# Performance work log

Measured on AMD Instinct MI355X. Metric: run time of the kernel, lower is better.

## Reference

```python
import jax, jax.numpy as jnp
import numpy as np


def lut_quantize(v, lut):
    """Nearest-neighbor LUT quantization with straight-through estimator.
    lut is sorted ascending; uses searchsorted (no [N, L] blowup)."""
    L = lut.shape[0]
    idx = jnp.clip(jnp.searchsorted(lut, v), 1, L - 1)
    left = jnp.take(lut, idx - 1)
    right = jnp.take(lut, idx)
    q = jnp.where(v - left <= right - v, left, right)
    return v + jax.lax.stop_gradient(q - v)


def mem_conv(x, w, b, lut):
    # memConv2d: weights/bias snapped to LUT levels, then standard 3x3 SAME conv (NCHW/OIHW)
    wq = lut_quantize(w, lut)
    bq = lut_quantize(b, lut)
    y = jax.lax.conv_general_dilated(x, wq, window_strides=(1, 1),
                                     padding=((1, 1), (1, 1)),
                                     dimension_numbers=('NCHW', 'OIHW', 'NCHW'))
    return y + bq[None, :, None, None]


def mem_linear(x, w, b, lut):
    # memLinear: torch-style weight (out, in)
    return x @ lut_quantize(w, lut).T + lut_quantize(b, lut)


def mem_relu(x, lut):
    # memReLu: ReLU followed by LUT quantization of the activation
    return lut_quantize(jnp.maximum(x, 0.0), lut)


def max_pool_2x2(x):
    return jax.lax.reduce_window(x, -jnp.inf, jax.lax.max,
                                 (1, 1, 2, 2), (1, 1, 2, 2), 'VALID')


def _forward(x, lut, w1, b1, w2, b2, w3, b3, w4, b4, w5, b5, w6, b6,
             fw1, fb1, fw2, fb2, fw3, fb3):
    x = mem_relu(mem_conv(x, w1, b1, lut), lut)
    x = mem_relu(mem_conv(x, w2, b2, lut), lut)
    x = max_pool_2x2(x)                      # [B,32,16,16]
    x = mem_relu(mem_conv(x, w3, b3, lut), lut)
    x = mem_relu(mem_conv(x, w4, b4, lut), lut)
    x = max_pool_2x2(x)                      # [B,64,8,8]
    x = mem_relu(mem_conv(x, w5, b5, lut), lut)
    x = mem_relu(mem_conv(x, w6, b6, lut), lut)
    x = max_pool_2x2(x)                      # [B,128,4,4]
    x = x.reshape(-1, 128 * 4 * 4)
    x = mem_relu(mem_linear(x, fw1, fb1, lut), lut)
    x = mem_relu(mem_linear(x, fw2, fb2, lut), lut)
    x = mem_linear(x, fw3, fb3, lut)
    return jax.nn.softmax(x, axis=1)


def setup_inputs() -> dict:
    key = jax.random.key(0)
    ks = jax.random.split(key, 20)
    B = 512
    lut = jnp.linspace(-4.0, 4.0, 129).astype(jnp.float32)

    def conv_w(k, co, ci):
        scale = np.sqrt(2.0 / (ci * 9)).astype(np.float32)
        return jax.random.normal(k, (co, ci, 3, 3), jnp.float32) * scale

    def lin_w(k, co, ci):
        scale = np.sqrt(2.0 / ci).astype(np.float32)
        return jax.random.normal(k, (co, ci), jnp.float32) * scale

    return {
        'x': jax.random.normal(ks[0], (B, 3, 32, 32), jnp.float32),
        'lut': lut,
        'w1': conv_w(ks[1], 32, 3),   'b1': jnp.zeros((32,), jnp.float32),
        'w2': conv_w(ks[2], 32, 32),  'b2': jnp.zeros((32,), jnp.float32),
        'w3': conv_w(ks[3], 64, 32),  'b3': jnp.zeros((64,), jnp.float32),
        'w4': conv_w(ks[4], 64, 64),  'b4': jnp.zeros((64,), jnp.float32),
        'w5': conv_w(ks[5], 128, 64), 'b5': jnp.zeros((128,), jnp.float32),
        'w6': conv_w(ks[6], 128, 128),'b6': jnp.zeros((128,), jnp.float32),
        'fw1': lin_w(ks[7], 512, 2048), 'fb1': jnp.zeros((512,), jnp.float32),
        'fw2': lin_w(ks[8], 128, 512),  'fb2': jnp.zeros((128,), jnp.float32),
        'fw3': lin_w(ks[9], 10, 128),   'fb3': jnp.zeros((10,), jnp.float32),
    }


def reference(x, lut, w1, b1, w2, b2, w3, b3, w4, b4, w5, b5, w6, b6,
              fw1, fb1, fw2, fb2, fw3, fb3):
    return _forward(x, lut, w1, b1, w2, b2, w3, b3, w4, b4, w5, b5, w6, b6,
                    fw1, fb1, fw2, fb2, fw3, fb3)
```

## Files before the change

kernel.cpp:

```cpp
#include <hip/hip_runtime.h>
#include <cstddef>


#define B_SZ 512
typedef unsigned int u32;
typedef __attribute__((ext_vector_type(4))) int i32x4;

__device__ __forceinline__ float lutq(float v) {
    float k = ceilf(v * 16.0f - 0.5f);
    k = fminf(64.0f, fmaxf(-64.0f, k));
    return k * 0.0625f;
}
__device__ __forceinline__ int kq(float x) {
    float kf = ceilf(x * 16.0f - 0.5f);
    kf = fminf(64.0f, fmaxf(-64.0f, kf));
    return (int)kf;
}
__device__ __forceinline__ u32 bmax4u(u32 a, u32 b) {
    u32 r = 0;
    #pragma unroll
    for (int j = 0; j < 4; ++j) {
        u32 x = (a >> (8 * j)) & 255u, y = (b >> (8 * j)) & 255u;
        r |= (x > y ? x : y) << (8 * j);
    }
    return r;
}

__device__ __forceinline__ void prep_conv_frag(const float* __restrict__ w, char* __restrict__ q,
                                               int i, int CI) {
    int NSTEP = (9 * CI + 63) / 64;
    int e = i & 15, t = i >> 4;
    int ln = t & 63, t2 = t >> 6;
    int s = t2 % NSTEP, co_tile = t2 / NSTEP;
    int k = s * 64 + ((ln >> 4) << 4) + e;
    int tap = k / CI, ci = k % CI;
    int co = co_tile * 16 + (ln & 15);
    int val = 0;
    if (tap < 9) val = kq(w[(co * CI + ci) * 9 + tap]);
    q[i] = (char)val;
}
__device__ __forceinline__ void prep_fc_frag(const float* __restrict__ w, char* __restrict__ q,
                                             int i, int K) {
    int S = K >> 6;
    int e = i & 15, t = i >> 4;
    int ln = t & 63, t2 = t >> 6;
    int s = t2 % S, n_tile = t2 / S;
    int n = n_tile * 16 + (ln & 15);
    int k = s * 64 + ((ln >> 4) << 4) + e;
    q[i] = (char)kq(w[(size_t)n * K + k]);
}

__global__ __launch_bounds__(256) void prep_weights(
    const float* __restrict__ w2, const float* __restrict__ w3, const float* __restrict__ w4,
    const float* __restrict__ w5, const float* __restrict__ w6,
    const float* __restrict__ fw1, const float* __restrict__ fw2,
    char* q2, char* q3, char* q4, char* q5, char* q6, char* qf1, char* qf2)
{
    int i = blockIdx.x * 256 + threadIdx.x;
    if (i < 10240)                  { prep_conv_frag(w2, q2, i, 32);  }
    else if ((i -= 10240) < 20480)  { prep_conv_frag(w3, q3, i, 32);  }
    else if ((i -= 20480) < 36864)  { prep_conv_frag(w4, q4, i, 64);  }
    else if ((i -= 36864) < 73728)  { prep_conv_frag(w5, q5, i, 64);  }
    else if ((i -= 73728) < 147456) { prep_conv_frag(w6, q6, i, 128); }
    else if ((i -= 147456) < 1048576){ prep_fc_frag(fw1, qf1, i, 2048); }
    else if ((i -= 1048576) < 65536) { prep_fc_frag(fw2, qf2, i, 512);  }
}

__global__ __launch_bounds__(256) void conv1_mem(
    const float* __restrict__ x, const float* __restrict__ w,
    const float* __restrict__ bias, char* __restrict__ out)
{
    __shared__ float s_w[3][9][32];
    __shared__ float s_b[32];
    __shared__ float s_in[3][10][34];
    const int tid = threadIdx.x;
    const int b   = blockIdx.x >> 2;
    const int r0  = (blockIdx.x & 3) * 8;
    for (int i = tid; i < 864; i += 256) {
        int o = i % 32, k = (i / 32) % 9, c = i / 288;
        s_w[c][k][o] = lutq(w[(o * 3 + c) * 9 + k]);
    }
    if (tid < 32) s_b[tid] = lutq(bias[tid]);
    for (int i = tid; i < 3 * 10 * 34; i += 256) {
        int xx = i % 34, yy = (i / 34) % 10, c = i / 340;
        int gy = r0 + yy - 1, gx = xx - 1;
        float v = 0.f;
        if ((unsigned)gy < 32u && (unsigned)gx < 32u)
            v = x[(((size_t)b * 3 + c) * 32 + gy) * 32 + gx];
        s_in[c][yy][xx] = v;
    }
    __syncthreads();
    const int y = tid >> 5, xx = tid & 31;
    float acc[32];
    #pragma unroll
    for (int o = 0; o < 32; ++o) acc[o] = 0.f;
    #pragma unroll
    for (int c = 0; c < 3; ++c) {
        #pragma unroll
        for (int k = 0; k < 9; ++k) {
            float iv = s_in[c][y + k / 3][xx + k % 3];
            #pragma unroll
            for (int o = 0; o < 32; ++o) acc[o] = fmaf(iv, s_w[c][k][o], acc[o]);
        }
    }
    u32 u[8];
    #pragma unroll
    for (int j = 0; j < 8; ++j) {
        u32 p = 0;
        #pragma unroll
        for (int q = 0; q < 4; ++q) {
            float v = fmaxf(acc[4 * j + q] + s_b[4 * j + q], 0.f);
            int kk = (int)ceilf(v * 16.0f - 0.5f);
            kk = kk > 64 ? 64 : kk;
            p |= ((u32)kk & 255u) << (8 * q);
        }
        u[j] = p;
    }
    const int p = (b << 10) + ((r0 + y) << 5) + xx;
    u32* o4 = (u32*)(out + (size_t)p * 32);
    #pragma unroll
    for (int j = 0; j < 8; ++j) o4[j] = u[j];
}

template<int HW, int CI, int CO, int RS, int NIMG, int NT, int POOL = 0>
__global__ __launch_bounds__(256) void conv_mfma(
    const char* __restrict__ in,
    const char* __restrict__ wq,
    const float* __restrict__ bias,
    char* __restrict__ out)
{
    constexpr int PH  = HW + 2;
    constexpr int PIX = NIMG * (RS + 2) * PH;
    constexpr int M   = NIMG * RS * HW;
    constexpr int MT  = M / 16;
    constexpr int MW  = MT / 4;
    constexpr int NSTEP = (9 * CI + 63) / 64;
    constexpr int SL  = HW / RS;
    constexpr int NC16 = CI / 16;
    constexpr int NTC = NT * 16;

    __shared__ __align__(128) char s_in[PIX * CI];

    const int tid = threadIdx.x;
    const int g   = blockIdx.x;
    const int b0  = (g / SL) * NIMG;
    const int r0  = (g % SL) * RS;
    const int co0 = blockIdx.y * NTC;

    constexpr int TOTC = PIX * NC16;
    for (int i = tid; i < TOTC; i += 256) {
        int c16 = i % NC16;
        int pp  = i / NC16;
        int xx  = pp % PH;
        int rr  = pp / PH;
        int yy  = rr % (RS + 2);
        int img = rr / (RS + 2);
        int gy = r0 + yy - 1, gx = xx - 1;
        uint4 v = {0u, 0u, 0u, 0u};
        if ((unsigned)gy < (unsigned)HW && (unsigned)gx < (unsigned)HW)
            v = *(const uint4*)(in + ((((size_t)(b0 + img) * HW + gy) * HW + gx) * CI + c16 * 16));
        int off = (pp * CI + c16 * 16) ^ ((pp & 7) << 4);
        *(uint4*)(s_in + off) = v;
    }
    __syncthreads();

    const int wv = tid >> 6, ln = tid & 63;
    const int l15 = ln & 15, lq = ln >> 4;

    int ppad[MW];
    #pragma unroll
    for (int mw = 0; mw < MW; ++mw) {
        int p = (wv * MW + mw) * 16 + l15;
        int img = p / (RS * HW);
        int rem = p % (RS * HW);
        int ly = rem / HW, lx = rem % HW;
        ppad[mw] = (img * (RS + 2) + ly + 1) * PH + lx + 1;
    }

    i32x4 acc[MW][NT] = {};

    const char* wtile = wq + ((size_t)blockIdx.y * NT) * NSTEP * 1024 + (ln << 4);
    auto dp = [](int t) { return (t / 3 - 1) * PH + (t % 3 - 1); };

    #pragma unroll
    for (int s = 0; s < NSTEP; ++s) {
        i32x4 bf[NT];
        #pragma unroll
        for (int nt = 0; nt < NT; ++nt)
            bf[nt] = *(const i32x4*)(wtile + ((nt * NSTEP + s) << 10));
        int dd, ci0;
        if constexpr (CI == 32) {
            int d0 = dp(2 * s);
            int d1 = (2 * s + 1 < 9) ? dp(2 * s + 1) : 0;
            dd  = (lq & 2) ? d1 : d0;
            ci0 = (lq & 1) << 4;
        } else if constexpr (CI == 64) {
            dd  = dp(s);
            ci0 = lq << 4;
        } else {
            dd  = dp(s >> 1);
            ci0 = ((s & 1) << 6) + (lq << 4);
        }
        #pragma unroll
        for (int mw = 0; mw < MW; ++mw) {
            int pix = ppad[mw] + dd;
            int off = (pix * CI + ci0) ^ ((pix & 7) << 4);
            i32x4 af = *(const i32x4*)(s_in + off);
            #pragma unroll
            for (int nt = 0; nt < NT; ++nt)
                acc[mw][nt] = __builtin_amdgcn_mfma_i32_16x16x64_i8(af, bf[nt], acc[mw][nt], 0, 0, 0);
        }
    }

    if constexpr (POOL == 0) {
        #pragma unroll
        for (int nt = 0; nt < NT; ++nt) {
            int kb16 = 16 * kq(bias[co0 + nt * 16 + l15]);
            #pragma unroll
            for (int mw = 0; mw < MW; ++mw) {
                #pragma unroll
                for (int r = 0; r < 4; ++r) {
                    int p = (wv * MW + mw) * 16 + lq * 4 + r;
                    int img = p / (RS * HW), rem = p % (RS * HW);
                    int ly = rem / HW, lx = rem % HW;
                    int vv = acc[mw][nt][r] + kb16;
                    vv = vv > 0 ? vv : 0;
                    int kk = (vv + 7) >> 4;
                    kk = kk > 64 ? 64 : kk;
                    out[(((size_t)(b0 + img) * HW + r0 + ly) * HW + lx) * CO + co0 + nt * 16 + l15] = (char)kk;
                }
            }
        }
    } else {
        __syncthreads();
        char* s_out = s_in;
        #pragma unroll
        for (int nt = 0; nt < NT; ++nt) {
            int kb16 = 16 * kq(bias[co0 + nt * 16 + l15]);
            #pragma unroll
            for (int mw = 0; mw < MW; ++mw) {
                #pragma unroll
                for (int r = 0; r < 4; ++r) {
                    int p = (wv * MW + mw) * 16 + lq * 4 + r;
                    int vv = acc[mw][nt][r] + kb16;
                    vv = vv > 0 ? vv : 0;
                    int kk = (vv + 7) >> 4;
                    kk = kk > 64 ? 64 : kk;
                    s_out[p * NTC + nt * 16 + l15] = (char)kk;
                }
            }
        }
        __syncthreads();
        constexpr int PR = RS / 2, PC = HW / 2, HOW = HW / 2;
        constexpr int OCT = NIMG * PR * PC * (NTC / 16);
        for (int idx = tid; idx < OCT; idx += 256) {
            int c16 = idx % (NTC / 16);
            int pp  = idx / (NTC / 16);
            int xo = pp % PC, yo = (pp / PC) % PR, img = pp / (PC * PR);
            int pb = (img * RS + 2 * yo) * HW + 2 * xo;
            uint4 v0 = *(const uint4*)(s_out + (pb)          * NTC + c16 * 16);
            uint4 v1 = *(const uint4*)(s_out + (pb + 1)      * NTC + c16 * 16);
            uint4 v2 = *(const uint4*)(s_out + (pb + HW)     * NTC + c16 * 16);
            uint4 v3 = *(const uint4*)(s_out + (pb + HW + 1) * NTC + c16 * 16);
            uint4 r;
            r.x = bmax4u(bmax4u(v0.x, v1.x), bmax4u(v2.x, v3.x));
            r.y = bmax4u(bmax4u(v0.y, v1.y), bmax4u(v2.y, v3.y));
            r.z = bmax4u(bmax4u(v0.z, v1.z), bmax4u(v2.z, v3.z));
            r.w = bmax4u(bmax4u(v0.w, v1.w), bmax4u(v2.w, v3.w));
            if constexpr (POOL == 1) {
                *(uint4*)(out + ((((size_t)(b0 + img) * HOW + (r0 >> 1) + yo) * HOW + xo) * CO
                                 + co0 + c16 * 16)) = r;
            } else {
                const char* rv = (const char*)&r;
                int m = b0 + img;
                #pragma unroll
                for (int j = 0; j < 16; ++j) {
                    int c = co0 + c16 * 16 + j;
                    int k = c * 16 + yo * 4 + xo;
                    int off = (((m >> 4) * 32 + (k >> 6)) << 10)
                            + ((((k >> 4) & 3) * 16 + (m & 15)) << 4) + (k & 15);
                    out[off] = rv[j];
                }
            }
        }
    }
}

template<int N, int K, int SK>
__global__ __launch_bounds__(256) void fc1_splitk(
    const char* __restrict__ xa, const char* __restrict__ wq, int* __restrict__ part)
{
    constexpr int KCH = K / SK;
    constexpr int KS = K / 64;
    const int tid = threadIdx.x, wv = tid >> 6, ln = tid & 63;
    const int l15 = ln & 15, lq = ln >> 4;
    const int m0 = blockIdx.x * 128, n0 = blockIdx.y * 128;
    const int kb = blockIdx.z * KCH;
    const int mq = (wv >> 1) * 4, nq = (wv & 1) * 4;
    i32x4 acc[4][4] = {};
    const char* xr[4];
    const char* wt[4];
    #pragma unroll
    for (int t = 0; t < 4; ++t) {
        xr[t] = xa + (size_t)((m0 >> 4) + mq + t) * KS * 1024 + (ln << 4);
        wt[t] = wq + (size_t)((n0 >> 4) + nq + t) * KS * 1024 + (ln << 4);
    }
    for (int k0 = 0; k0 < KCH; k0 += 64) {
        const int s = (kb + k0) >> 6;
        i32x4 a[4], b[4];
        #pragma unroll
        for (int t = 0; t < 4; ++t) {
            a[t] = *(const i32x4*)(xr[t] + (s << 10));
            b[t] = *(const i32x4*)(wt[t] + (s << 10));
        }
        #pragma unroll
        for (int i = 0; i < 4; ++i)
            #pragma unroll
            for (int j = 0; j < 4; ++j)
                acc[i][j] = __builtin_amdgcn_mfma_i32_16x16x64_i8(a[i], b[j], acc[i][j], 0, 0, 0);
    }
    int* pb = part + (size_t)blockIdx.z * (B_SZ * N);
    #pragma unroll
    for (int j = 0; j < 4; ++j) {
        int n = n0 + (nq + j) * 16 + l15;
        #pragma unroll
        for (int i = 0; i < 4; ++i)
            #pragma unroll
            for (int r = 0; r < 4; ++r) {
                int m = m0 + (mq + i) * 16 + lq * 4 + r;
                pb[(size_t)m * N + n] = acc[i][j][r];
            }
    }
}

template<int N, int SK>
__global__ __launch_bounds__(256) void fc_reduce(
    const int* __restrict__ part, const float* __restrict__ bias, char* __restrict__ out)
{
    int i = blockIdx.x * 256 + threadIdx.x;
    if (i >= B_SZ * N) return;
    int s = 0;
    #pragma unroll
    for (int k = 0; k < SK; ++k) s += part[(size_t)k * (B_SZ * N) + i];
    int vv = s + 16 * kq(bias[i % N]);
    vv = vv > 0 ? vv : 0;
    int kk = (vv + 7) >> 4;
    kk = kk > 64 ? 64 : kk;
    out[i] = (char)kk;
}

__global__ __launch_bounds__(256) void fc_tail(
    const char* __restrict__ x, const char* __restrict__ qf2,
    const float* __restrict__ fb2, const float* __restrict__ fw3,
    const float* __restrict__ fb3, float* __restrict__ out)
{
    __shared__ __align__(16) char sx[32 * 512];
    __shared__ __align__(16) char sy[32 * 128];
    __shared__ __align__(16) char sw3[10 * 128];
    __shared__ float sb3[10];
    __shared__ int sp[32][8][10];

    const int tid = threadIdx.x;
    const int m0 = blockIdx.x * 32;

    for (int idx = tid; idx < 1024; idx += 256) {
        int r = idx >> 5, c16 = idx & 31;
        uint4 v = *(const uint4*)(x + (size_t)(m0 + r) * 512 + c16 * 16);
        *(uint4*)(sx + ((r * 512 + c16 * 16) ^ ((r & 7) << 4))) = v;
    }
    for (int i = tid; i < 1280; i += 256) sw3[i] = (char)kq(fw3[i]);
    if (tid < 10) sb3[tid] = lutq(fb3[tid]);
    __syncthreads();

    const int wv = tid >> 6, ln = tid & 63, l15 = ln & 15, lq = ln >> 4;
    const int mt = wv >> 1, ntg = (wv & 1) * 4;
    i32x4 acc[4] = {};
    #pragma unroll
    for (int s = 0; s < 8; ++s) {
        int row = mt * 16 + l15;
        i32x4 a = *(const i32x4*)(sx + ((row * 512 + s * 64 + lq * 16) ^ ((row & 7) << 4)));
        #pragma unroll
        for (int nt = 0; nt < 4; ++nt) {
            i32x4 b = *(const i32x4*)(qf2 + (((ntg + nt) * 8 + s) << 10) + (ln << 4));
            acc[nt] = __builtin_amdgcn_mfma_i32_16x16x64_i8(a, b, acc[nt], 0, 0, 0);
        }
    }
    #pragma unroll
    for (int nt = 0; nt < 4; ++nt) {
        int n = (ntg + nt) * 16 + l15;
        int kb16 = 16 * kq(fb2[n]);
        #pragma unroll
        for (int r = 0; r < 4; ++r) {
            int row = mt * 16 + lq * 4 + r;
            int vv = acc[nt][r] + kb16;
            vv = vv > 0 ? vv : 0;
            int kk = (vv + 7) >> 4;
            kk = kk > 64 ? 64 : kk;
            sy[(row * 128 + n) ^ ((row & 7) << 4)] = (char)kk;
        }
    }
    __syncthreads();

    {
        int r = tid >> 3, g = tid & 7;
        uint4 yv = *(const uint4*)(sy + ((r * 128 + g * 16) ^ ((r & 7) << 4)));
        const char* yb = (const char*)&yv;
        #pragma unroll
        for (int o = 0; o < 10; ++o) {
            uint4 wv4 = *(const uint4*)(sw3 + o * 128 + g * 16);
            const char* wb = (const char*)&wv4;
            int S = 0;
            #pragma unroll
            for (int e = 0; e < 16; ++e) S += (int)yb[e] * (int)wb[e];
            sp[r][g][o] = S;
        }
    }
    __syncthreads();

    if (tid < 32) {
        int r = tid;
        float d[10];
        #pragma unroll
        for (int o = 0; o < 10; ++o) {
            int S = 0;
            #pragma unroll
            for (int g = 0; g < 8; ++g) S += sp[r][g][o];
            d[o] = (float)S * 0.00390625f + sb3[o];
        }
        float m = d[0];
        #pragma unroll
        for (int o = 1; o < 10; ++o) m = fmaxf(m, d[o]);
        float e[10];
        float sum = 0.f;
        #pragma unroll
        for (int o = 0; o < 10; ++o) { e[o] = expf(d[o] - m); sum += e[o]; }
        #pragma unroll
        for (int o = 0; o < 10; ++o) out[(size_t)(m0 + r) * 10 + o] = e[o] / sum;
    }
}

extern "C" void kernel_launch(void* const* d_in, const int* in_sizes, int n_in,
                              void* d_out, int out_size, void* d_ws, size_t ws_size,
                              hipStream_t stream)
{
    const float* x   = (const float*)d_in[0];
    const float* w1  = (const float*)d_in[2];
    const float* b1  = (const float*)d_in[3];
    const float* w2  = (const float*)d_in[4];
    const float* b2  = (const float*)d_in[5];
    const float* w3  = (const float*)d_in[6];
    const float* b3  = (const float*)d_in[7];
    const float* w4  = (const float*)d_in[8];
    const float* b4  = (const float*)d_in[9];
    const float* w5  = (const float*)d_in[10];
    const float* b5  = (const float*)d_in[11];
    const float* w6  = (const float*)d_in[12];
    const float* b6  = (const float*)d_in[13];
    const float* fw1 = (const float*)d_in[14];
    const float* fb1 = (const float*)d_in[15];
    const float* fw2 = (const float*)d_in[16];
    const float* fb2 = (const float*)d_in[17];
    const float* fw3 = (const float*)d_in[18];
    const float* fb3 = (const float*)d_in[19];
    float* out = (float*)d_out;

    char* bufA = (char*)d_ws;
    char* bufB = bufA + (16u << 20);
    char* q2  = bufB + (16u << 20);
    char* q3  = q2 + 10240;
    char* q4  = q3 + 20480;
    char* q5  = q4 + 36864;
    char* q6  = q5 + 73728;
    char* qf1 = q6 + 147456;
    char* qf2 = qf1 + 1048576;
    int*  part = (int*)(qf2 + 65536);
    char* fc1out = (char*)part + (16u << 20);
    char* fc1a   = fc1out + 262144;

    dim3 blk(256);

    prep_weights<<<dim3((1402880 + 255) / 256), blk, 0, stream>>>(
        w2, w3, w4, w5, w6, fw1, fw2, q2, q3, q4, q5, q6, qf1, qf2);

    conv1_mem<<<dim3(2048), blk, 0, stream>>>(x, w1, b1, bufA);
    conv_mfma<32, 32, 32, 8, 1, 2, 1><<<dim3(2048, 1), blk, 0, stream>>>(bufA, q2, b2, bufB);
    conv_mfma<16, 32, 64, 16, 1, 4, 0><<<dim3(512, 1), blk, 0, stream>>>(bufB, q3, b3, bufA);
    conv_mfma<16, 64, 64, 16, 1, 4, 1><<<dim3(512, 1), blk, 0, stream>>>(bufA, q4, b4, bufB);
    conv_mfma<8, 64, 128, 8, 2, 4, 0><<<dim3(256, 2), blk, 0, stream>>>(bufB, q5, b5, bufA);
    conv_mfma<8, 128, 128, 8, 2, 4, 2><<<dim3(256, 2), blk, 0, stream>>>(bufA, q6, b6, fc1a);

    fc1_splitk<512, 2048, 16><<<dim3(4, 4, 16), blk, 0, stream>>>(fc1a, qf1, part);
    fc_reduce<512, 16><<<dim3(1024), blk, 0, stream>>>(part, fb1, fc1out);
    fc_tail<<<dim3(16), blk, 0, stream>>>(fc1out, qf2, fb2, fw3, fb3, out);
}
```

Measured before the change: 97.62 us.

## Merge weight prep with conv1, drop split-K for fc1, halve fc_tail tile

Weight quantization and conv1 now run in one launch, with block ranges dispatching to either job. The fc1 GEMM no longer splits K 16 ways: each of 16 blocks runs the full K loop and applies bias, ReLU and quantization itself, so the partial-sum buffer and the reduce kernel are gone. fc_tail uses 16-row tiles across 32 blocks to spread the tail work over more CUs. The cost is that fc1 runs on only 16 blocks with long serial K loops, which may underuse the GPU.

```diff
diff --git a/kernel.cpp b/kernel.cpp
--- a/kernel.cpp
+++ b/kernel.cpp
@@ -50,37 +50,38 @@
     q[i] = (char)kq(w[(size_t)n * K + k]);
 }
 
-__global__ __launch_bounds__(256) void prep_weights(
+__global__ __launch_bounds__(256) void prep_conv1(
     const float* __restrict__ w2, const float* __restrict__ w3, const float* __restrict__ w4,
     const float* __restrict__ w5, const float* __restrict__ w6,
     const float* __restrict__ fw1, const float* __restrict__ fw2,
-    char* q2, char* q3, char* q4, char* q5, char* q6, char* qf1, char* qf2)
+    char* q2, char* q3, char* q4, char* q5, char* q6, char* qf1, char* qf2,
+    const float* __restrict__ x, const float* __restrict__ w1,
+    const float* __restrict__ b1, char* __restrict__ out)
 {
-    int i = blockIdx.x * 256 + threadIdx.x;
-    if (i < 10240)                  { prep_conv_frag(w2, q2, i, 32);  }
-    else if ((i -= 10240) < 20480)  { prep_conv_frag(w3, q3, i, 32);  }
-    else if ((i -= 20480) < 36864)  { prep_conv_frag(w4, q4, i, 64);  }
-    else if ((i -= 36864) < 73728)  { prep_conv_frag(w5, q5, i, 64);  }
-    else if ((i -= 73728) < 147456) { prep_conv_frag(w6, q6, i, 128); }
-    else if ((i -= 147456) < 1048576){ prep_fc_frag(fw1, qf1, i, 2048); }
-    else if ((i -= 1048576) < 65536) { prep_fc_frag(fw2, qf2, i, 512);  }
-}
-
-__global__ __launch_bounds__(256) void conv1_mem(
-    const float* __restrict__ x, const float* __restrict__ w,
-    const float* __restrict__ bias, char* __restrict__ out)
-{
+    const int tid = threadIdx.x;
+    const int bid = blockIdx.x;
+    if (bid < 5480) {
+        int i = bid * 256 + tid;
+        if (i < 10240)                  { prep_conv_frag(w2, q2, i, 32);  }
+        else if ((i -= 10240) < 20480)  { prep_conv_frag(w3, q3, i, 32);  }
+        else if ((i -= 20480) < 36864)  { prep_conv_frag(w4, q4, i, 64);  }
+        else if ((i -= 36864) < 73728)  { prep_conv_frag(w5, q5, i, 64);  }
+        else if ((i -= 73728) < 147456) { prep_conv_frag(w6, q6, i, 128); }
+        else if ((i -= 147456) < 1048576){ prep_fc_frag(fw1, qf1, i, 2048); }
+        else if ((i -= 1048576) < 65536) { prep_fc_frag(fw2, qf2, i, 512);  }
+        return;
+    }
     __shared__ float s_w[3][9][32];
     __shared__ float s_b[32];
     __shared__ float s_in[3][10][34];
-    const int tid = threadIdx.x;
-    const int b   = blockIdx.x >> 2;
-    const int r0  = (blockIdx.x & 3) * 8;
+    const int bx  = bid - 5480;
+    const int b   = bx >> 2;
+    const int r0  = (bx & 3) * 8;
     for (int i = tid; i < 864; i += 256) {
         int o = i % 32, k = (i / 32) % 9, c = i / 288;
-        s_w[c][k][o] = lutq(w[(o * 3 + c) * 9 + k]);
-    }
-    if (tid < 32) s_b[tid] = lutq(bias[tid]);
+        s_w[c][k][o] = lutq(w1[(o * 3 + c) * 9 + k]);
+    }
+    if (tid < 32) s_b[tid] = lutq(b1[tid]);
     for (int i = tid; i < 3 * 10 * 34; i += 256) {
         int xx = i % 34, yy = (i / 34) % 10, c = i / 340;
         int gy = r0 + yy - 1, gx = xx - 1;
@@ -286,16 +287,14 @@
     }
 }
 
-template<int N, int K, int SK>
-__global__ __launch_bounds__(256) void fc1_splitk(
-    const char* __restrict__ xa, const char* __restrict__ wq, int* __restrict__ part)
+__global__ __launch_bounds__(256) void fc1_mfma(
+    const char* __restrict__ xa, const char* __restrict__ wq,
+    const float* __restrict__ bias, char* __restrict__ out)
 {
-    constexpr int KCH = K / SK;
-    constexpr int KS = K / 64;
+    constexpr int KS = 2048 / 64;
     const int tid = threadIdx.x, wv = tid >> 6, ln = tid & 63;
     const int l15 = ln & 15, lq = ln >> 4;
     const int m0 = blockIdx.x * 128, n0 = blockIdx.y * 128;
-    const int kb = blockIdx.z * KCH;
     const int mq = (wv >> 1) * 4, nq = (wv & 1) * 4;
     i32x4 acc[4][4] = {};
     const char* xr[4];
@@ -305,8 +304,8 @@
         xr[t] = xa + (size_t)((m0 >> 4) + mq + t) * KS * 1024 + (ln << 4);
         wt[t] = wq + (size_t)((n0 >> 4) + nq + t) * KS * 1024 + (ln << 4);
     }
-    for (int k0 = 0; k0 < KCH; k0 += 64) {
-        const int s = (kb + k0) >> 6;
+    #pragma unroll 4
+    for (int s = 0; s < KS; ++s) {
         i32x4 a[4], b[4];
         #pragma unroll
         for (int t = 0; t < 4; ++t) {
@@ -319,34 +318,22 @@
             for (int j = 0; j < 4; ++j)
                 acc[i][j] = __builtin_amdgcn_mfma_i32_16x16x64_i8(a[i], b[j], acc[i][j], 0, 0, 0);
     }
-    int* pb = part + (size_t)blockIdx.z * (B_SZ * N);
     #pragma unroll
     for (int j = 0; j < 4; ++j) {
         int n = n0 + (nq + j) * 16 + l15;
+        int kb16 = 16 * kq(bias[n]);
         #pragma unroll
         for (int i = 0; i < 4; ++i)
             #pragma unroll
             for (int r = 0; r < 4; ++r) {
                 int m = m0 + (mq + i) * 16 + lq * 4 + r;
-                pb[(size_t)m * N + n] = acc[i][j][r];
+                int vv = acc[i][j][r] + kb16;
+                vv = vv > 0 ? vv : 0;
+                int kk = (vv + 7) >> 4;
+                kk = kk > 64 ? 64 : kk;
+                out[(size_t)m * 512 + n] = (char)kk;
             }
     }
-}
-
-template<int N, int SK>
-__global__ __launch_bounds__(256) void fc_reduce(
-    const int* __restrict__ part, const float* __restrict__ bias, char* __restrict__ out)
-{
-    int i = blockIdx.x * 256 + threadIdx.x;
-    if (i >= B_SZ * N) return;
-    int s = 0;
-    #pragma unroll
-    for (int k = 0; k < SK; ++k) s += part[(size_t)k * (B_SZ * N) + i];
-    int vv = s + 16 * kq(bias[i % N]);
-    vv = vv > 0 ? vv : 0;
-    int kk = (vv + 7) >> 4;
-    kk = kk > 64 ? 64 : kk;
-    out[i] = (char)kk;
 }
 
 __global__ __launch_bounds__(256) void fc_tail(
@@ -354,16 +341,16 @@
     const float* __restrict__ fb2, const float* __restrict__ fw3,
     const float* __restrict__ fb3, float* __restrict__ out)
 {
-    __shared__ __align__(16) char sx[32 * 512];
-    __shared__ __align__(16) char sy[32 * 128];
+    __shared__ __align__(16) char sx[16 * 512];
+    __shared__ __align__(16) char sy[16 * 128];
     __shared__ __align__(16) char sw3[10 * 128];
     __shared__ float sb3[10];
-    __shared__ int sp[32][8][10];
+    __shared__ int sp[16][16][10];
 
     const int tid = threadIdx.x;
-    const int m0 = blockIdx.x * 32;
-
-    for (int idx = tid; idx < 1024; idx += 256) {
+    const int m0 = blockIdx.x * 16;
+
+    for (int idx = tid; idx < 512; idx += 256) {
         int r = idx >> 5, c16 = idx & 31;
         uint4 v = *(const uint4*)(x + (size_t)(m0 + r) * 512 + c16 * 16);
         *(uint4*)(sx + ((r * 512 + c16 * 16) ^ ((r & 7) << 4))) = v;
@@ -373,25 +360,25 @@
     __syncthreads();
 
     const int wv = tid >> 6, ln = tid & 63, l15 = ln & 15, lq = ln >> 4;
-    const int mt = wv >> 1, ntg = (wv & 1) * 4;
-    i32x4 acc[4] = {};
+    const int ntg = wv * 2;
+    i32x4 acc[2] = {};
     #pragma unroll
     for (int s = 0; s < 8; ++s) {
-        int row = mt * 16 + l15;
+        int row = l15;
         i32x4 a = *(const i32x4*)(sx + ((row * 512 + s * 64 + lq * 16) ^ ((row & 7) << 4)));
         #pragma unroll
-        for (int nt = 0; nt < 4; ++nt) {
+        for (int nt = 0; nt < 2; ++nt) {
             i32x4 b = *(const i32x4*)(qf2 + (((ntg + nt) * 8 + s) << 10) + (ln << 4));
             acc[nt] = __builtin_amdgcn_mfma_i32_16x16x64_i8(a, b, acc[nt], 0, 0, 0);
         }
     }
     #pragma unroll
-    for (int nt = 0; nt < 4; ++nt) {
+    for (int nt = 0; nt < 2; ++nt) {
         int n = (ntg + nt) * 16 + l15;
         int kb16 = 16 * kq(fb2[n]);
         #pragma unroll
         for (int r = 0; r < 4; ++r) {
-            int row = mt * 16 + lq * 4 + r;
+            int row = lq * 4 + r;
             int vv = acc[nt][r] + kb16;
             vv = vv > 0 ? vv : 0;
             int kk = (vv + 7) >> 4;
@@ -402,29 +389,29 @@
     __syncthreads();
 
     {
-        int r = tid >> 3, g = tid & 7;
-        uint4 yv = *(const uint4*)(sy + ((r * 128 + g * 16) ^ ((r & 7) << 4)));
+        int r = tid >> 4, g = tid & 15;
+        uint2 yv = *(const uint2*)(sy + ((r * 128 + g * 8) ^ ((r & 7) << 4)));
         const char* yb = (const char*)&yv;
         #pragma unroll
         for (int o = 0; o < 10; ++o) {
-            uint4 wv4 = *(const uint4*)(sw3 + o * 128 + g * 16);
-            const char* wb = (const char*)&wv4;
+            uint2 wv2 = *(const uint2*)(sw3 + o * 128 + g * 8);
+            const char* wb = (const char*)&wv2;
             int S = 0;
             #pragma unroll
-            for (int e = 0; e < 16; ++e) S += (int)yb[e] * (int)wb[e];
+            for (int e = 0; e < 8; ++e) S += (int)yb[e] * (int)wb[e];
             sp[r][g][o] = S;
         }
     }
     __syncthreads();
 
-    if (tid < 32) {
+    if (tid < 16) {
         int r = tid;
         float d[10];
         #pragma unroll
         for (int o = 0; o < 10; ++o) {
             int S = 0;
             #pragma unroll
-            for (int g = 0; g < 8; ++g) S += sp[r][g][o];
+            for (int g = 0; g < 16; ++g) S += sp[r][g][o];
             d[o] = (float)S * 0.00390625f + sb3[o];
         }
         float m = d[0];
@@ -473,23 +460,19 @@
     char* q6  = q5 + 73728;
     char* qf1 = q6 + 147456;
     char* qf2 = qf1 + 1048576;
-    int*  part = (int*)(qf2 + 65536);
-    char* fc1out = (char*)part + (16u << 20);
+    char* fc1out = qf2 + 65536;
     char* fc1a   = fc1out + 262144;
 
     dim3 blk(256);
 
-    prep_weights<<<dim3((1402880 + 255) / 256), blk, 0, stream>>>(
-        w2, w3, w4, w5, w6, fw1, fw2, q2, q3, q4, q5, q6, qf1, qf2);
-
-    conv1_mem<<<dim3(2048), blk, 0, stream>>>(x, w1, b1, bufA);
+    prep_conv1<<<dim3(7528), blk, 0, stream>>>(
+        w2, w3, w4, w5, w6, fw1, fw2, q2, q3, q4, q5, q6, qf1, qf2,
+        x, w1, b1, bufA);
     conv_mfma<32, 32, 32, 8, 1, 2, 1><<<dim3(2048, 1), blk, 0, stream>>>(bufA, q2, b2, bufB);
     conv_mfma<16, 32, 64, 16, 1, 4, 0><<<dim3(512, 1), blk, 0, stream>>>(bufB, q3, b3, bufA);
     conv_mfma<16, 64, 64, 16, 1, 4, 1><<<dim3(512, 1), blk, 0, stream>>>(bufA, q4, b4, bufB);
     conv_mfma<8, 64, 128, 8, 2, 4, 0><<<dim3(256, 2), blk, 0, stream>>>(bufB, q5, b5, bufA);
     conv_mfma<8, 128, 128, 8, 2, 4, 2><<<dim3(256, 2), blk, 0, stream>>>(bufA, q6, b6, fc1a);
-
-    fc1_splitk<512, 2048, 16><<<dim3(4, 4, 16), blk, 0, stream>>>(fc1a, qf1, part);
-    fc_reduce<512, 16><<<dim3(1024), blk, 0, stream>>>(part, fb1, fc1out);
-    fc_tail<<<dim3(16), blk, 0, stream>>>(fc1out, qf2, fb2, fw3, fb3, out);
-}
+    fc1_mfma<<<dim3(4, 4), blk, 0, stream>>>(fc1a, qf1, fb1, fc1out);
+    fc_tail<<<dim3(32), blk, 0, stream>>>(fc1out, qf2, fb2, fw3, fb3, out);
+}
```

Result: slower. 109.6 us (+12.2%).
